# Performance work log

Measured on AMD Instinct MI355X. Metric: run time of the kernel, lower is better.

Reference implementation:

```python
import jax, jax.numpy as jnp
import numpy as np

B, S, H, D = 4, 2048, 16, 128
E = H * D  # emb_dim = 2048


def setup_inputs() -> dict:
    key = jax.random.key(0)
    ks = jax.random.split(key, 9)
    s_in = 1.0 / np.sqrt(E)
    return {
        "inputs": jax.random.normal(ks[0], (B, S, E), dtype=jnp.float32),
        "Wq": jax.random.normal(ks[1], (E, E), dtype=jnp.float32) * s_in,
        "bq": jnp.zeros((E,), dtype=jnp.float32),
        "Wk": jax.random.normal(ks[2], (E, E), dtype=jnp.float32) * s_in,
        "bk": jnp.zeros((E,), dtype=jnp.float32),
        "Wv": jax.random.normal(ks[3], (E, E), dtype=jnp.float32) * s_in,
        "bv": jnp.zeros((E,), dtype=jnp.float32),
        "Wo": jax.random.normal(ks[4], (E, E), dtype=jnp.float32) * s_in,
        "bo": jnp.zeros((E,), dtype=jnp.float32),
    }


def reference(inputs, Wq, bq, Wk, bk, Wv, bv, Wo, bo):
    b, s, e = inputs.shape
    # QKV projections -> [B, H, S, D]
    q = (inputs @ Wq + bq).reshape(b, s, H, D).transpose(0, 2, 1, 3)
    k = (inputs @ Wk + bk).reshape(b, s, H, D).transpose(0, 2, 1, 3)
    v = (inputs @ Wv + bv).reshape(b, s, H, D).transpose(0, 2, 1, 3)
    scale = 1.0 / jnp.sqrt(jnp.asarray(D, dtype=q.dtype))
    # Scaled dot-product attention (what the blockwise flash loop computes)
    scores = jnp.einsum('bhqd,bhkd->bhqk', q, k) * scale
    probs = jax.nn.softmax(scores, axis=-1)
    attn = jnp.einsum('bhqk,bhkd->bhqd', probs, v)
    attn = attn.transpose(0, 2, 1, 3).reshape(b, s, e)
    return attn @ Wo + bo
```

## Files before the change

### kernel.cpp

```cpp
#include <hip/hip_runtime.h>
#include <hip/hip_bf16.h>
#include <stdint.h>

typedef __bf16 bf16;
typedef float f32x4 __attribute__((ext_vector_type(4)));
typedef bf16 bf16x4 __attribute__((ext_vector_type(4)));
typedef bf16 bf16x8 __attribute__((ext_vector_type(8)));

#define DEV __device__ __forceinline__

DEV void gload16(const void* g, void* l) {
  __builtin_amdgcn_global_load_lds((const __attribute__((address_space(1))) void*)g,
                                   (__attribute__((address_space(3))) void*)l, 16, 0, 0);
}

DEV f32x4 mfma16(bf16x8 a, bf16x8 b, f32x4 c) {
  return __builtin_amdgcn_mfma_f32_16x16x32_bf16(a, b, c, 0, 0, 0);
}

#if __has_builtin(__builtin_amdgcn_exp2f)
DEV float EXP2F(float x) { return __builtin_amdgcn_exp2f(x); }
#else
DEV float EXP2F(float x) { return exp2f(x); }
#endif

static constexpr int Bn = 4, Sn = 2048, Hn = 16, Dn = 128, En = 2048, Mn = 8192;

__global__ void prep(const float* __restrict__ X, bf16* __restrict__ Xb,
                     const float* __restrict__ Wq, const float* __restrict__ Wk,
                     const float* __restrict__ Wv, const float* __restrict__ Wo,
                     bf16* __restrict__ Wqt, bf16* __restrict__ Wkt,
                     bf16* __restrict__ Wvt, bf16* __restrict__ Wot, int n8) {
  __shared__ bf16 t[64][65];
  const int bid = blockIdx.x;
  if (bid < 2048) {
    int i = bid * 256 + threadIdx.x;
    const int stride = 2048 * 256;
    for (int idx = i; idx < n8; idx += stride) {
      const float4* p = (const float4*)(X + (size_t)idx * 8);
      float4 a = p[0], b = p[1];
      bf16x8 o;
      o[0]=(bf16)a.x; o[1]=(bf16)a.y; o[2]=(bf16)a.z; o[3]=(bf16)a.w;
      o[4]=(bf16)b.x; o[5]=(bf16)b.y; o[6]=(bf16)b.z; o[7]=(bf16)b.w;
      *(bf16x8*)(Xb + (size_t)idx * 8) = o;
    }
    return;
  }
  const int q = bid - 2048;
  const int mtx = q >> 10, within = q & 1023;
  const float* W = (mtx == 0) ? Wq : (mtx == 1) ? Wk : (mtx == 2) ? Wv : Wo;
  bf16* Wt = (mtx == 0) ? Wqt : (mtx == 1) ? Wkt : (mtx == 2) ? Wvt : Wot;
  int tx = threadIdx.x & 15, ty = threadIdx.x >> 4;
  int c0 = (within & 31) * 64, r0 = (within >> 5) * 64;
  #pragma unroll
  for (int i = 0; i < 4; ++i) {
    int r = i * 16 + ty;
    float4 v = *(const float4*)&W[(size_t)(r0 + r) * En + c0 + tx * 4];
    t[r][tx*4+0] = (bf16)v.x; t[r][tx*4+1] = (bf16)v.y;
    t[r][tx*4+2] = (bf16)v.z; t[r][tx*4+3] = (bf16)v.w;
  }
  __syncthreads();
  #pragma unroll
  for (int i = 0; i < 4; ++i) {
    int c = i * 16 + ty;
    bf16x4 o;
    #pragma unroll
    for (int j = 0; j < 4; ++j) o[j] = t[tx*4+j][c];
    *(bf16x4*)&Wt[(size_t)(c0 + c) * En + r0 + tx * 4] = o;
  }
}

#define STAGE_A(H, DBUF, KTN) do { \
    const bf16* s_ = A + (size_t)(mbase + (tid >> 2)) * K + (KTN) * 64 + (H) * 32 \
                     + (((tid & 3) ^ ((tid >> 3) & 3)) * 8); \
    uint8_t* d_ = (DBUF) + (H) * 16384 + (w << 10); \
    gload16(s_, d_); \
    gload16(s_ + (size_t)128 * K, d_ + 8192); \
  } while (0)
#define STAGE_B(H, DBUF, KTN) do { \
    const bf16* s_ = Bt + (size_t)(nbase + (tid >> 2)) * K + (KTN) * 64 + (H) * 32 \
                     + (((tid & 3) ^ ((tid >> 3) & 3)) * 8); \
    uint8_t* d_ = (DBUF) + (H) * 16384 + (w << 10); \
    gload16(s_, d_); \
    gload16(s_ + (size_t)128 * K, d_ + 8192); \
  } while (0)

template<int OUT_MODE>
__global__ __launch_bounds__(512, 2) void gemm256(
    const bf16* __restrict__ A, const bf16* __restrict__ Bt,
    const float* __restrict__ b0, const float* __restrict__ b1,
    const float* __restrict__ b2, void* __restrict__ Cout,
    bf16* __restrict__ Vout,
    int M, int N, int K, int sbx, int sby)
{
  __shared__ __align__(16) uint8_t smem[131072];
  const int tid = threadIdx.x, lane = tid & 63, w = tid >> 6;
  const int wm = w >> 2, wn = w & 3;
  const int g = lane >> 4, lr = lane & 15;
  const int gx = (g ^ ((lr >> 1) & 3)) << 4;
  const int lid = blockIdx.x;
  const int xcd = lid & 7, i = lid >> 3;
  const int bx = (xcd & 1) * sbx + (i % sbx);
  const int by = (xcd >> 1) * sby + (i / sbx);
  const int mbase = by * 256, nbase = bx * 256;

  f32x4 acc[8][4] = {};

  STAGE_A(0, smem, 0);
  STAGE_B(0, smem + 65536, 0);
  STAGE_A(1, smem, 0);
  STAGE_B(1, smem + 65536, 0);
  asm volatile("s_waitcnt vmcnt(0)" ::: "memory");
  __builtin_amdgcn_s_barrier();

  const int NKT = K >> 6;
  for (int kt = 0; kt < NKT; ++kt) {
    const int cur = kt & 1;
    uint8_t* Acur = smem + (cur << 15);
    uint8_t* Bcur = smem + 65536 + (cur << 15);
    uint8_t* Anxt = smem + ((cur ^ 1) << 15);
    uint8_t* Bnxt = smem + 65536 + ((cur ^ 1) << 15);
    const bool notlast = (kt + 1 < NKT);

    if (notlast) {
      STAGE_A(0, Anxt, kt + 1);
      STAGE_B(0, Bnxt, kt + 1);
      STAGE_A(1, Anxt, kt + 1);
      STAGE_B(1, Bnxt, kt + 1);
    }

    bf16x8 a0[8], b0v[4], a1[8], b1v[4];
    #pragma unroll
    for (int mf = 0; mf < 8; ++mf)
      a0[mf] = *(const bf16x8*)(Acur + (wm * 128 + mf * 16 + lr) * 64 + gx);
    #pragma unroll
    for (int j = 0; j < 4; ++j)
      b0v[j] = *(const bf16x8*)(Bcur + (wn * 64 + j * 16 + lr) * 64 + gx);
    #pragma unroll
    for (int mf = 0; mf < 8; ++mf)
      a1[mf] = *(const bf16x8*)(Acur + 16384 + (wm * 128 + mf * 16 + lr) * 64 + gx);
    #pragma unroll
    for (int j = 0; j < 4; ++j)
      b1v[j] = *(const bf16x8*)(Bcur + 16384 + (wn * 64 + j * 16 + lr) * 64 + gx);

    __builtin_amdgcn_s_setprio(1);
    #pragma unroll
    for (int mf = 0; mf < 8; ++mf)
      #pragma unroll
      for (int j = 0; j < 4; ++j)
        acc[mf][j] = mfma16(a0[mf], b0v[j], acc[mf][j]);
    #pragma unroll
    for (int mf = 0; mf < 8; ++mf)
      #pragma unroll
      for (int j = 0; j < 4; ++j)
        acc[mf][j] = mfma16(a1[mf], b1v[j], acc[mf][j]);
    __builtin_amdgcn_s_setprio(0);

    asm volatile("s_waitcnt vmcnt(0)" ::: "memory");
    __builtin_amdgcn_s_barrier();
  }

  if constexpr (OUT_MODE == 0) {
    int tsel = nbase >> 11;
    if (tsel == 2) {
      #pragma unroll
      for (int j = 0; j < 4; ++j) {
        int nn = (nbase + wn * 64 + j * 16 + lr) & 2047;
        int h = nn >> 7, d = nn & 127;
        float bv = b2[nn];
        #pragma unroll
        for (int mf = 0; mf < 8; ++mf) {
          int m0 = mbase + wm * 128 + mf * 16 + g * 4;
          int b = m0 >> 11, s0 = m0 & 2047;
          bf16x4 o4;
          #pragma unroll
          for (int r = 0; r < 4; ++r) o4[r] = (bf16)(acc[mf][j][r] + bv);
          *(bf16x4*)&Vout[((size_t)(b * Hn + h) * Dn + d) * Sn + s0] = o4;
        }
      }
    } else {
      const float* bsel = (tsel == 0) ? b0 : b1;
      #pragma unroll
      for (int j = 0; j < 4; ++j) {
        int n = nbase + wn * 64 + j * 16 + lr;
        int nn = n & 2047;
        float bv = bsel[nn];
        int h = nn >> 7, d = nn & 127;
        #pragma unroll
        for (int mf = 0; mf < 8; ++mf) {
          #pragma unroll
          for (int r = 0; r < 4; ++r) {
            int m = mbase + wm * 128 + mf * 16 + g * 4 + r;
            int b = m >> 11, s = m & 2047;
            ((bf16*)Cout)[(size_t)tsel * ((size_t)Mn * En) +
                          ((size_t)(b * Hn + h) * Sn + s) * Dn + d] = (bf16)(acc[mf][j][r] + bv);
          }
        }
      }
    }
  } else {
    #pragma unroll
    for (int j = 0; j < 4; ++j) {
      int n = nbase + wn * 64 + j * 16 + lr;
      float bv = b0[n];
      #pragma unroll
      for (int mf = 0; mf < 8; ++mf) {
        #pragma unroll
        for (int r = 0; r < 4; ++r) {
          int m = mbase + wm * 128 + mf * 16 + g * 4 + r;
          ((float*)Cout)[(size_t)m * N + n] = acc[mf][j][r] + bv;
        }
      }
    }
  }
}

__global__ __launch_bounds__(512, 2) void attn(
    const bf16* __restrict__ Q, const bf16* __restrict__ K,
    const bf16* __restrict__ Vt, bf16* __restrict__ O)
{
  __shared__ __align__(16) uint8_t smem[65536];
  const int tid = threadIdx.x, lane = tid & 63, w = tid >> 6;
  const int g = lane >> 4, lr = lane & 15;
  const int lid = blockIdx.x;
  const int xcd = lid & 7, j = lid >> 3;
  const int bh = xcd * 8 + (j >> 3);
  const int q0 = (j & 7) * 256;
  const size_t hoff = (size_t)bh * Sn * Dn;
  const bf16* Qh = Q + hoff;
  const bf16* Kh = K + hoff;
  const bf16* Vh = Vt + hoff;
  const float SC2 = 0.12751744f;

  #pragma unroll
  for (int it = 0; it < 8; ++it) {
    int cl = it * 512 + tid;
    int row = cl >> 4, cs = cl & 15;
    int cg = cs ^ (row & 7);
    gload16(Qh + (size_t)(q0 + row) * Dn + cg * 8, smem + (it * 512 + (tid & ~63)) * 16);
  }
  __syncthreads();
  bf16x8 qf[2][4];
  #pragma unroll
  for (int nf = 0; nf < 2; ++nf)
    #pragma unroll
    for (int ks = 0; ks < 4; ++ks) {
      int row = w * 32 + nf * 16 + lr;
      qf[nf][ks] = *(const bf16x8*)(smem + row * 256 + (((ks * 4 + g) ^ (row & 7)) << 4));
    }
  __syncthreads();

  const int vd = tid >> 2, vq = tid & 3;
  const bf16* vrow = Vh + (size_t)vd * Sn + (vq >> 1) * 32 + (vq & 1) * 8;

  uint4 u0, u1;
  #pragma unroll
  for (int it = 0; it < 2; ++it) {
    int cl = it * 512 + tid;
    int row = cl >> 4, cs = cl & 15;
    int cg = cs ^ (row & 7);
    gload16(Kh + (size_t)row * Dn + cg * 8, smem + (it * 512 + (tid & ~63)) * 16);
  }
  { const uint4* vs = (const uint4*)vrow; u0 = vs[0]; u1 = vs[2]; }

  f32x4 o[2][8] = {};
  float m2[2] = { -__builtin_inff(), -__builtin_inff() };
  float lrun[2] = { 0.f, 0.f };

  for (int t = 0; t < 32; ++t) {
    const int cur = t & 1;
    uint8_t* Kcur = smem + (cur << 14);
    uint8_t* Knxt = smem + ((cur ^ 1) << 14);
    uint8_t* Vcur = smem + 32768 + (cur << 14);
    asm volatile("s_waitcnt vmcnt(0)" ::: "memory");
    {
      uint8_t* base = Vcur + vd * 128;
      const int sw = vd & 7;
      *(uint4*)(base + (((2 * vq + 0) ^ sw) << 4)) = make_uint4(u0.x, u0.y, u1.x, u1.y);
      *(uint4*)(base + (((2 * vq + 1) ^ sw) << 4)) = make_uint4(u0.z, u0.w, u1.z, u1.w);
    }
    if (t < 31) {
      const int kvn = (t + 1) * 64;
      #pragma unroll
      for (int it = 0; it < 2; ++it) {
        int cl = it * 512 + tid;
        int row = cl >> 4, cs = cl & 15;
        int cg = cs ^ (row & 7);
        gload16(Kh + (size_t)(kvn + row) * Dn + cg * 8,
                Knxt + (it * 512 + (tid & ~63)) * 16);
      }
      const uint4* vs = (const uint4*)(vrow + kvn);
      u0 = vs[0]; u1 = vs[2];
    }
    asm volatile("s_waitcnt lgkmcnt(0)" ::: "memory");
    asm volatile("s_barrier" ::: "memory");

    f32x4 sfr[2][4] = {};
    __builtin_amdgcn_s_setprio(1);
    #pragma unroll
    for (int ks = 0; ks < 4; ++ks) {
      #pragma unroll
      for (int mf = 0; mf < 4; ++mf) {
        int row = mf * 16 + lr;
        bf16x8 kf = *(const bf16x8*)(Kcur + row * 256 + (((ks * 4 + g) ^ (row & 7)) << 4));
        sfr[0][mf] = mfma16(kf, qf[0][ks], sfr[0][mf]);
        sfr[1][mf] = mfma16(kf, qf[1][ks], sfr[1][mf]);
      }
    }
    __builtin_amdgcn_s_setprio(0);

    bf16x8 pa[2][2];
    #pragma unroll
    for (int nf = 0; nf < 2; ++nf) {
      f32x4 a0, a1;
      #pragma unroll
      for (int r = 0; r < 4; ++r) a0[r] = fmaxf(sfr[nf][0][r], sfr[nf][1][r]);
      #pragma unroll
      for (int r = 0; r < 4; ++r) a1[r] = fmaxf(sfr[nf][2][r], sfr[nf][3][r]);
      #pragma unroll
      for (int r = 0; r < 4; ++r) a0[r] = fmaxf(a0[r], a1[r]);
      float mx = fmaxf(fmaxf(a0[0], a0[1]), fmaxf(a0[2], a0[3]));
      mx = fmaxf(mx, __shfl_xor(mx, 16));
      mx = fmaxf(mx, __shfl_xor(mx, 32));
      float pm2 = mx * SC2;
      if (__any(pm2 > m2[nf] + 8.f)) {
        float mnew = fmaxf(m2[nf], pm2);
        float fsc = EXP2F(m2[nf] - mnew);
        m2[nf] = mnew;
        lrun[nf] *= fsc;
        float fv[4];
        #pragma unroll
        for (int r = 0; r < 4; ++r) fv[r] = __shfl(fsc, g * 4 + r);
        #pragma unroll
        for (int df = 0; df < 8; ++df)
          #pragma unroll
          for (int r = 0; r < 4; ++r) o[nf][df][r] *= fv[r];
      }
      const float mc = m2[nf];
      f32x4 p[4];
      #pragma unroll
      for (int mf = 0; mf < 4; ++mf)
        #pragma unroll
        for (int r = 0; r < 4; ++r)
          p[mf][r] = EXP2F(__builtin_fmaf(sfr[nf][mf][r], SC2, -mc));
      f32x4 s0, s1;
      #pragma unroll
      for (int r = 0; r < 4; ++r) s0[r] = p[0][r] + p[1][r];
      #pragma unroll
      for (int r = 0; r < 4; ++r) s1[r] = p[2][r] + p[3][r];
      #pragma unroll
      for (int r = 0; r < 4; ++r) s0[r] += s1[r];
      float ps = (s0[0] + s0[1]) + (s0[2] + s0[3]);
      ps += __shfl_xor(ps, 16);
      ps += __shfl_xor(ps, 32);
      lrun[nf] += ps;
      #pragma unroll
      for (int ks = 0; ks < 2; ++ks) {
        bf16x8 tt;
        #pragma unroll
        for (int i = 0; i < 4; ++i) {
          tt[i]     = (bf16)p[2 * ks][i];
          tt[i + 4] = (bf16)p[2 * ks + 1][i];
        }
        pa[nf][ks] = tt;
      }
    }

    __builtin_amdgcn_s_setprio(1);
    #pragma unroll
    for (int ks = 0; ks < 2; ++ks) {
      #pragma unroll
      for (int df = 0; df < 8; ++df) {
        int row = df * 16 + lr;
        bf16x8 vf = *(const bf16x8*)(Vcur + row * 128 + (((ks * 4 + g) ^ (row & 7)) << 4));
        o[0][df] = mfma16(pa[0][ks], vf, o[0][df]);
        o[1][df] = mfma16(pa[1][ks], vf, o[1][df]);
      }
    }
    __builtin_amdgcn_s_setprio(0);
    asm volatile("s_barrier" ::: "memory");
  }

  const int b = bh >> 4, h = bh & 15;
  #pragma unroll
  for (int nf = 0; nf < 2; ++nf) {
    float inv = 1.f / lrun[nf];
    float iv[4];
    #pragma unroll
    for (int r = 0; r < 4; ++r) iv[r] = __shfl(inv, g * 4 + r);
    #pragma unroll
    for (int df = 0; df < 8; ++df) {
      #pragma unroll
      for (int r = 0; r < 4; ++r) {
        int qrow = q0 + w * 32 + nf * 16 + g * 4 + r;
        int d = df * 16 + lr;
        size_t m = (size_t)b * Sn + qrow;
        O[m * En + h * Dn + d] = (bf16)(o[nf][df][r] * iv[r]);
      }
    }
  }
}

extern "C" void kernel_launch(void* const* d_in, const int* in_sizes, int n_in,
                              void* d_out, int out_size, void* d_ws, size_t ws_size,
                              hipStream_t stream) {
  const float* X  = (const float*)d_in[0];
  const float* Wq = (const float*)d_in[1];
  const float* bq = (const float*)d_in[2];
  const float* Wk = (const float*)d_in[3];
  const float* bk = (const float*)d_in[4];
  const float* Wv = (const float*)d_in[5];
  const float* bv = (const float*)d_in[6];
  const float* Wo = (const float*)d_in[7];
  const float* bo = (const float*)d_in[8];

  bf16* ws = (bf16*)d_ws;
  const size_t szE = (size_t)Mn * En;
  const size_t szW = (size_t)En * En;
  bf16* Xb  = ws;
  bf16* Wqt = Xb + szE;
  bf16* Wkt = Wqt + szW;
  bf16* Wvt = Wkt + szW;
  bf16* Wot = Wvt + szW;
  bf16* Qb  = Wot + szW;
  bf16* Kb  = Qb + szE;
  bf16* Vb  = Kb + szE;
  bf16* Vtp = Vb + szE;
  bf16* AO  = Vb;

  prep<<<6144, 256, 0, stream>>>(X, Xb, Wq, Wk, Wv, Wo, Wqt, Wkt, Wvt, Wot,
                                 (int)(szE / 8));
  gemm256<0><<<768, 512, 0, stream>>>(Xb, Wqt, bq, bk, bv, Qb, Vtp,
                                      Mn, 3 * En, En, 12, 8);
  attn<<<512, 512, 0, stream>>>(Qb, Kb, Vtp, AO);
  gemm256<1><<<256, 512, 0, stream>>>(AO, Wot, bo, nullptr, nullptr, d_out, nullptr,
                                      Mn, En, En, 4, 8);
}
```

Baseline: 461.9 us.

## Load A operand fragments directly from global memory instead of staging through LDS

The GEMM kernel now reads A fragments straight from global memory into registers each k-step. Only the B tile goes through the LDS double buffer, which halves LDS usage to 64KB. This removes LDS write/read traffic for A and may allow higher occupancy. In exchange the A loads are uncoalesced, strided per row, and no longer prefetched a stage ahead, so global load latency is exposed right before the MFMAs, and each A element is re-read by the four wn waves.

```diff
diff --git a/kernel.cpp b/kernel.cpp
--- a/kernel.cpp
+++ b/kernel.cpp
@@ -70,13 +70,6 @@
   }
 }
 
-#define STAGE_A(H, DBUF, KTN) do { \
-    const bf16* s_ = A + (size_t)(mbase + (tid >> 2)) * K + (KTN) * 64 + (H) * 32 \
-                     + (((tid & 3) ^ ((tid >> 3) & 3)) * 8); \
-    uint8_t* d_ = (DBUF) + (H) * 16384 + (w << 10); \
-    gload16(s_, d_); \
-    gload16(s_ + (size_t)128 * K, d_ + 8192); \
-  } while (0)
 #define STAGE_B(H, DBUF, KTN) do { \
     const bf16* s_ = Bt + (size_t)(nbase + (tid >> 2)) * K + (KTN) * 64 + (H) * 32 \
                      + (((tid & 3) ^ ((tid >> 3) & 3)) * 8); \
@@ -93,7 +86,7 @@
     bf16* __restrict__ Vout,
     int M, int N, int K, int sbx, int sby)
 {
-  __shared__ __align__(16) uint8_t smem[131072];
+  __shared__ __align__(16) uint8_t smem[65536];
   const int tid = threadIdx.x, lane = tid & 63, w = tid >> 6;
   const int wm = w >> 2, wn = w & 3;
   const int g = lane >> 4, lr = lane & 15;
@@ -104,41 +97,41 @@
   const int by = (xcd >> 1) * sby + (i / sbx);
   const int mbase = by * 256, nbase = bx * 256;
 
+  const bf16* Abase = A + (size_t)(mbase + wm * 128 + lr) * K + g * 8;
+  const int rowstride = 16 * K;
+
   f32x4 acc[8][4] = {};
 
-  STAGE_A(0, smem, 0);
-  STAGE_B(0, smem + 65536, 0);
-  STAGE_A(1, smem, 0);
-  STAGE_B(1, smem + 65536, 0);
+  STAGE_B(0, smem, 0);
+  STAGE_B(1, smem, 0);
   asm volatile("s_waitcnt vmcnt(0)" ::: "memory");
   __builtin_amdgcn_s_barrier();
 
   const int NKT = K >> 6;
   for (int kt = 0; kt < NKT; ++kt) {
     const int cur = kt & 1;
-    uint8_t* Acur = smem + (cur << 15);
-    uint8_t* Bcur = smem + 65536 + (cur << 15);
-    uint8_t* Anxt = smem + ((cur ^ 1) << 15);
-    uint8_t* Bnxt = smem + 65536 + ((cur ^ 1) << 15);
+    uint8_t* Bcur = smem + (cur << 15);
+    uint8_t* Bnxt = smem + ((cur ^ 1) << 15);
     const bool notlast = (kt + 1 < NKT);
 
+    const bf16* Ak = Abase + kt * 64;
+    bf16x8 a0[8], a1[8];
+    #pragma unroll
+    for (int mf = 0; mf < 8; ++mf)
+      a0[mf] = *(const bf16x8*)(Ak + mf * rowstride);
+    #pragma unroll
+    for (int mf = 0; mf < 8; ++mf)
+      a1[mf] = *(const bf16x8*)(Ak + mf * rowstride + 32);
+
     if (notlast) {
-      STAGE_A(0, Anxt, kt + 1);
       STAGE_B(0, Bnxt, kt + 1);
-      STAGE_A(1, Anxt, kt + 1);
       STAGE_B(1, Bnxt, kt + 1);
     }
 
-    bf16x8 a0[8], b0v[4], a1[8], b1v[4];
-    #pragma unroll
-    for (int mf = 0; mf < 8; ++mf)
-      a0[mf] = *(const bf16x8*)(Acur + (wm * 128 + mf * 16 + lr) * 64 + gx);
+    bf16x8 b0v[4], b1v[4];
     #pragma unroll
     for (int j = 0; j < 4; ++j)
       b0v[j] = *(const bf16x8*)(Bcur + (wn * 64 + j * 16 + lr) * 64 + gx);
-    #pragma unroll
-    for (int mf = 0; mf < 8; ++mf)
-      a1[mf] = *(const bf16x8*)(Acur + 16384 + (wm * 128 + mf * 16 + lr) * 64 + gx);
     #pragma unroll
     for (int j = 0; j < 4; ++j)
       b1v[j] = *(const bf16x8*)(Bcur + 16384 + (wn * 64 + j * 16 + lr) * 64 + gx);
```

After: 839.6 us. +81.8%, slower.
